# Optimization experiments

Measured on AMD Instinct MI355X. Metric: run time of the kernel, lower is better.

Reference implementation:

```python
import math
import jax, jax.numpy as jnp
import numpy as np

D = 512; H = 8; N = 6; DFF = 2048; VS = 32000; VT = 32000
B = 4; S = 1024; T = 1024
EPS = 1e-5


def _pe(length, d):
    pos = jnp.arange(length, dtype=jnp.float32)[:, None]
    div = jnp.exp(jnp.arange(0, d, 2, dtype=jnp.float32) * (-math.log(10000.0) / d))
    pe = jnp.zeros((length, d), jnp.float32)
    pe = pe.at[:, 0::2].set(jnp.sin(pos * div)).at[:, 1::2].set(jnp.cos(pos * div))
    return pe  # [L, D]


def _ln(x, g, b):
    m = x.mean(-1, keepdims=True)
    v = ((x - m) ** 2).mean(-1, keepdims=True)
    return (x - m) / jnp.sqrt(v + EPS) * g + b


def _mha(xq, xkv, w, b, mask):
    # w: [4, D, D], b: [4, D]; mask broadcastable to [B, H, Sq, Sk]
    nb, sq, d = xq.shape
    dk = d // H
    def proj(x, i):
        return (x @ w[i] + b[i]).reshape(x.shape[0], x.shape[1], H, dk).transpose(0, 2, 1, 3)
    q, k, v = proj(xq, 0), proj(xkv, 1), proj(xkv, 2)
    scores = jnp.einsum('bhqd,bhkd->bhqk', q, k) / math.sqrt(dk)
    scores = jnp.where(mask == 0, -1e9, scores)
    p = jax.nn.softmax(scores, axis=-1)
    o = jnp.einsum('bhqk,bhkd->bhqd', p, v).transpose(0, 2, 1, 3).reshape(nb, sq, d)
    return o @ w[3] + b[3]


def _ffn(x, w1, b1, w2, b2):
    return jax.nn.relu(x @ w1 + b1) @ w2 + b2


def _forward(src_emb, tgt_emb,
             enc_attn_w, enc_attn_b, enc_ffn_w1, enc_ffn_b1, enc_ffn_w2, enc_ffn_b2,
             enc_ln_g, enc_ln_b, enc_fg, enc_fb,
             dec_self_w, dec_self_b, dec_src_w, dec_src_b,
             dec_ffn_w1, dec_ffn_b1, dec_ffn_w2, dec_ffn_b2,
             dec_ln_g, dec_ln_b, dec_fg, dec_fb,
             gen_w, gen_b,
             src, tgt, src_mask, tgt_mask):
    # embed + positional encoding (dropout off: eval mode)
    x = src_emb[src] + _pe(src.shape[1], D)[None]
    for i in range(N):
        a = _mha(x, x, enc_attn_w[i], enc_attn_b[i], src_mask)
        x = _ln(x + a, enc_ln_g[i, 0], enc_ln_b[i, 0])
        f = _ffn(x, enc_ffn_w1[i], enc_ffn_b1[i], enc_ffn_w2[i], enc_ffn_b2[i])
        x = _ln(x + f, enc_ln_g[i, 1], enc_ln_b[i, 1])
    memory = _ln(x, enc_fg, enc_fb)

    y = tgt_emb[tgt] + _pe(tgt.shape[1], D)[None]
    for i in range(N):
        a = _mha(y, y, dec_self_w[i], dec_self_b[i], tgt_mask)
        y = _ln(y + a, dec_ln_g[i, 0], dec_ln_b[i, 0])
        a = _mha(y, memory, dec_src_w[i], dec_src_b[i], src_mask)
        y = _ln(y + a, dec_ln_g[i, 1], dec_ln_b[i, 1])
        f = _ffn(y, dec_ffn_w1[i], dec_ffn_b1[i], dec_ffn_w2[i], dec_ffn_b2[i])
        y = _ln(y + f, dec_ln_g[i, 2], dec_ln_b[i, 2])
    y = _ln(y, dec_fg, dec_fb)
    return y @ gen_w + gen_b  # [B, T, VT]


def setup_inputs():
    key = jax.random.key(0)
    ks = iter(jax.random.split(key, 48))
    def w(*shape):
        return jax.random.normal(next(ks), shape, dtype=jnp.float32) * 0.02
    inp = {}
    inp['src_emb'] = w(VS, D)
    inp['tgt_emb'] = w(VT, D)
    inp['enc_attn_w'] = w(N, 4, D, D)
    inp['enc_attn_b'] = jnp.zeros((N, 4, D), jnp.float32)
    inp['enc_ffn_w1'] = w(N, D, DFF)
    inp['enc_ffn_b1'] = jnp.zeros((N, DFF), jnp.float32)
    inp['enc_ffn_w2'] = w(N, DFF, D)
    inp['enc_ffn_b2'] = jnp.zeros((N, D), jnp.float32)
    inp['enc_ln_g'] = jnp.ones((N, 2, D), jnp.float32)
    inp['enc_ln_b'] = jnp.zeros((N, 2, D), jnp.float32)
    inp['enc_fg'] = jnp.ones((D,), jnp.float32)
    inp['enc_fb'] = jnp.zeros((D,), jnp.float32)
    inp['dec_self_w'] = w(N, 4, D, D)
    inp['dec_self_b'] = jnp.zeros((N, 4, D), jnp.float32)
    inp['dec_src_w'] = w(N, 4, D, D)
    inp['dec_src_b'] = jnp.zeros((N, 4, D), jnp.float32)
    inp['dec_ffn_w1'] = w(N, D, DFF)
    inp['dec_ffn_b1'] = jnp.zeros((N, DFF), jnp.float32)
    inp['dec_ffn_w2'] = w(N, DFF, D)
    inp['dec_ffn_b2'] = jnp.zeros((N, D), jnp.float32)
    inp['dec_ln_g'] = jnp.ones((N, 3, D), jnp.float32)
    inp['dec_ln_b'] = jnp.zeros((N, 3, D), jnp.float32)
    inp['dec_fg'] = jnp.ones((D,), jnp.float32)
    inp['dec_fb'] = jnp.zeros((D,), jnp.float32)
    inp['gen_w'] = w(D, VT)
    inp['gen_b'] = jnp.zeros((VT,), jnp.float32)
    inp['src'] = jax.random.randint(next(ks), (B, S), 0, VS)
    inp['tgt'] = jax.random.randint(next(ks), (B, T), 0, VT)
    inp['src_mask'] = jnp.ones((B, 1, 1, S), jnp.int32)
    inp['tgt_mask'] = jnp.tril(jnp.ones((T, T), jnp.int32))[None, None]  # causal [1,1,T,T]
    return inp


def reference(src_emb, tgt_emb, enc_attn_w, enc_attn_b, enc_ffn_w1, enc_ffn_b1,
              enc_ffn_w2, enc_ffn_b2, enc_ln_g, enc_ln_b, enc_fg, enc_fb,
              dec_self_w, dec_self_b, dec_src_w, dec_src_b,
              dec_ffn_w1, dec_ffn_b1, dec_ffn_w2, dec_ffn_b2,
              dec_ln_g, dec_ln_b, dec_fg, dec_fb, gen_w, gen_b,
              src, tgt, src_mask, tgt_mask):
    return _forward(src_emb, tgt_emb, enc_attn_w, enc_attn_b, enc_ffn_w1, enc_ffn_b1,
                    enc_ffn_w2, enc_ffn_b2, enc_ln_g, enc_ln_b, enc_fg, enc_fb,
                    dec_self_w, dec_self_b, dec_src_w, dec_src_b,
                    dec_ffn_w1, dec_ffn_b1, dec_ffn_w2, dec_ffn_b2,
                    dec_ln_g, dec_ln_b, dec_fg, dec_fb, gen_w, gen_b,
                    src, tgt, src_mask, tgt_mask)
```

## Files before the change

### kernel.cpp

```cpp
#include <hip/hip_runtime.h>


typedef __bf16 bf16x8 __attribute__((ext_vector_type(8)));
typedef __bf16 bf16x4 __attribute__((ext_vector_type(4)));
typedef float  f32x4  __attribute__((ext_vector_type(4)));

__device__ __forceinline__ void gload_lds16(const void* g, void* l) {
  __builtin_amdgcn_global_load_lds((__attribute__((address_space(1))) void*)g,
                                   (__attribute__((address_space(3))) void*)l,
                                   16, 0, 0);
}

__device__ __forceinline__ void hard_barrier() {
  asm volatile("" ::: "memory");
  __builtin_amdgcn_sched_barrier(0);
  __builtin_amdgcn_s_barrier();
  __builtin_amdgcn_sched_barrier(0);
  asm volatile("" ::: "memory");
}

template<int EPI>
__global__ __launch_bounds__(256)
void gemm2_kernel(const __bf16* __restrict__ A, int lda,
                  const __bf16* __restrict__ BT, int ldb,
                  void* __restrict__ Cv, int ldc,
                  const float* __restrict__ bias, int K,
                  __bf16* __restrict__ qb, __bf16* __restrict__ kb,
                  __bf16* __restrict__ vt, int zoff)
{
  constexpr int BM = 128, BN = 128, BK = 64;
  constexpr int WM = 64, WN = 64, FM = 4, FN = 4;
  constexpr int SLOT = 2 * BM * BK;
  __shared__ char ldsraw[69632];
  __bf16* lds = (__bf16*)ldsraw;
  const int tid  = threadIdx.x;
  const int lane = tid & 63, wave = tid >> 6;
  const int wr = wave >> 1, wc = wave & 1;
  const int bm = blockIdx.x * BM, bn = blockIdx.y * BN;

  auto stage = [&](int slot, int kt) {
    const char* Ag = (const char*)A;
    const char* Bg = (const char*)BT;
    char* base = (char*)(lds + slot * SLOT);
    const long long k0b = (long long)kt * (BK * 2);
#pragma unroll
    for (int i = 0; i < 4; i++) {
      int t = tid + i * 256;
      int row = t >> 3, cb = (t & 7) << 4;
      int src = cb ^ ((row & 7) << 4);
      gload_lds16(Ag + ((long long)(bm + row) * lda) * 2 + k0b + src, base + t * 16);
    }
#pragma unroll
    for (int i = 0; i < 4; i++) {
      int t = tid + i * 256;
      int row = t >> 3, cb = (t & 7) << 4;
      int src = cb ^ ((row & 7) << 4);
      gload_lds16(Bg + ((long long)(bn + row) * ldb) * 2 + k0b + src,
                  base + BM * BK * 2 + t * 16);
    }
  };

  f32x4 acc[FM][FN] = {};
  const int NT = K / BK;

  stage(0, 0);
  stage(1, 1);

  for (int t = 0; t < NT; t++) {
    if (t < NT - 1) {
      asm volatile("s_waitcnt vmcnt(8)" ::: "memory");
    } else {
      asm volatile("s_waitcnt vmcnt(0)" ::: "memory");
    }
    hard_barrier();
    const char* sA = (const char*)(lds + (t & 1) * SLOT);
    const char* sB = sA + BM * BK * 2;
#pragma unroll
    for (int kk = 0; kk < 2; kk++) {
      const int g = kk * 64 + (lane >> 4) * 16;
      bf16x8 af[FM], bfr[FN];
#pragma unroll
      for (int i = 0; i < FM; i++) {
        int row = wr * WM + i * 16 + (lane & 15);
        af[i] = *(const bf16x8*)(sA + row * 128 + (g ^ ((row & 7) << 4)));
      }
#pragma unroll
      for (int j = 0; j < FN; j++) {
        int row = wc * WN + j * 16 + (lane & 15);
        bfr[j] = *(const bf16x8*)(sB + row * 128 + (g ^ ((row & 7) << 4)));
      }
      __builtin_amdgcn_s_setprio(1);
#pragma unroll
      for (int i = 0; i < FM; i++)
#pragma unroll
        for (int j = 0; j < FN; j++)
          acc[i][j] = __builtin_amdgcn_mfma_f32_16x16x32_bf16(af[i], bfr[j], acc[i][j], 0, 0, 0);
      __builtin_amdgcn_s_setprio(0);
    }
    hard_barrier();
    if (t + 2 < NT) stage(t & 1, t + 2);
  }

  if constexpr (EPI == 3) {
    __syncthreads();
    float* ct = (float*)ldsraw;
#pragma unroll
    for (int i = 0; i < FM; i++) {
#pragma unroll
      for (int j = 0; j < FN; j++) {
        int lrow = wr * WM + i * 16 + (lane >> 4) * 4;
        int lcol = wc * WN + j * 16 + (lane & 15);
        float bv = bias[bn + lcol];
#pragma unroll
        for (int r = 0; r < 4; r++)
          ct[(lrow + r) * 132 + lcol] = acc[i][j][r] + bv;
      }
    }
    __syncthreads();
    float* C = (float*)Cv;
#pragma unroll
    for (int it = 0; it < 16; it++) {
      int idx = tid + it * 256;
      int row = idx >> 5, c4 = (idx & 31) * 4;
      f32x4 v = *(const f32x4*)(ct + row * 132 + c4);
      *(f32x4*)(C + (long long)(bm + row) * ldc + bn + c4) = v;
    }
    return;
  }

#pragma unroll
  for (int i = 0; i < FM; i++) {
#pragma unroll
    for (int j = 0; j < FN; j++) {
      int row0 = bm + wr * WM + i * 16 + (lane >> 4) * 4;
      int col  = bn + wc * WN + j * 16 + (lane & 15);
      float bv = bias ? bias[col] : 0.f;
      if constexpr (EPI == 2) {
        int z = zoff + (col >> 9);
        int cw = col & 511;
        int b = row0 >> 10, s = row0 & 1023;
        int h = cw >> 6, dk = cw & 63;
        long long bh = b * 8 + h;
        if (z == 2) {
          bf16x4 vv;
#pragma unroll
          for (int r = 0; r < 4; r++) vv[r] = (__bf16)(acc[i][j][r] + bv);
          *(bf16x4*)(vt + (bh << 16) + (dk << 10) + s) = vv;
        } else {
          __bf16* dst = (z == 0) ? qb : kb;
          float sc = (z == 0) ? 0.125f : 1.0f;
#pragma unroll
          for (int r = 0; r < 4; r++)
            dst[(bh << 16) + ((long long)(s + r) << 6) + dk] = (__bf16)((acc[i][j][r] + bv) * sc);
        }
      } else if constexpr (EPI == 1) {
        __bf16* C = (__bf16*)Cv;
#pragma unroll
        for (int r = 0; r < 4; r++)
          C[(long long)(row0 + r) * ldc + col] = (__bf16)fmaxf(acc[i][j][r] + bv, 0.f);
      } else {
        float* C = (float*)Cv;
#pragma unroll
        for (int r = 0; r < 4; r++)
          C[(long long)(row0 + r) * ldc + col] = acc[i][j][r] + bv;
      }
    }
  }
}

template<int EPI>
__global__ __launch_bounds__(256)
void gemm_kernel(const __bf16* __restrict__ A, int lda,
                 const __bf16* __restrict__ BT, int ldb,
                 void* __restrict__ Cv, int ldc,
                 const float* __restrict__ bias, int K,
                 __bf16* __restrict__ qb, __bf16* __restrict__ kb,
                 __bf16* __restrict__ vt, int zoff)
{
  constexpr int BM = 128, BN = 64, BK = 64;
  constexpr int WM = 64, WN = 32, FM = 4, FN = 2;
  constexpr int LA = (BM * BK) / 2048;
  constexpr int LB = (BN * BK) / 2048;
  constexpr int SLOT = (BM + BN) * BK;
  __shared__ __bf16 lds[3 * SLOT];
  const int tid  = threadIdx.x;
  const int lane = tid & 63, wave = tid >> 6;
  const int wr = wave >> 1, wc = wave & 1;
  const int bm = blockIdx.x * BM, bn = blockIdx.y * BN;

  auto stage = [&](int slot, int kt) {
    const char* Ag = (const char*)A;
    const char* Bg = (const char*)BT;
    char* base = (char*)(lds + slot * SLOT);
    const long long k0b = (long long)kt * (BK * 2);
#pragma unroll
    for (int i = 0; i < LA; i++) {
      int t = tid + i * 256;
      int row = t >> 3, cb = (t & 7) << 4;
      int src = cb ^ ((row & 7) << 4);
      gload_lds16(Ag + ((long long)(bm + row) * lda) * 2 + k0b + src, base + t * 16);
    }
#pragma unroll
    for (int i = 0; i < LB; i++) {
      int t = tid + i * 256;
      int row = t >> 3, cb = (t & 7) << 4;
      int src = cb ^ ((row & 7) << 4);
      gload_lds16(Bg + ((long long)(bn + row) * ldb) * 2 + k0b + src,
                  base + BM * BK * 2 + t * 16);
    }
  };

  f32x4 acc[FM][FN] = {};
  const int NT = K / BK;

  stage(0, 0);
  stage(1, 1);

  for (int t = 0; t < NT; t++) {
    if (t < NT - 1) {
      asm volatile("s_waitcnt vmcnt(6)" ::: "memory");
    } else {
      asm volatile("s_waitcnt vmcnt(0)" ::: "memory");
    }
    hard_barrier();
    if (t + 2 < NT) stage((t + 2) % 3, t + 2);
    const char* sA = (const char*)(lds + (t % 3) * SLOT);
    const char* sB = sA + BM * BK * 2;
#pragma unroll
    for (int kk = 0; kk < 2; kk++) {
      const int g = kk * 64 + (lane >> 4) * 16;
      bf16x8 af[FM], bfr[FN];
#pragma unroll
      for (int i = 0; i < FM; i++) {
        int row = wr * WM + i * 16 + (lane & 15);
        af[i] = *(const bf16x8*)(sA + row * 128 + (g ^ ((row & 7) << 4)));
      }
#pragma unroll
      for (int j = 0; j < FN; j++) {
        int row = wc * WN + j * 16 + (lane & 15);
        bfr[j] = *(const bf16x8*)(sB + row * 128 + (g ^ ((row & 7) << 4)));
      }
      __builtin_amdgcn_s_setprio(1);
#pragma unroll
      for (int i = 0; i < FM; i++)
#pragma unroll
        for (int j = 0; j < FN; j++)
          acc[i][j] = __builtin_amdgcn_mfma_f32_16x16x32_bf16(af[i], bfr[j], acc[i][j], 0, 0, 0);
      __builtin_amdgcn_s_setprio(0);
    }
  }

#pragma unroll
  for (int i = 0; i < FM; i++) {
#pragma unroll
    for (int j = 0; j < FN; j++) {
      int row0 = bm + wr * WM + i * 16 + (lane >> 4) * 4;
      int col  = bn + wc * WN + j * 16 + (lane & 15);
      float bv = bias ? bias[col] : 0.f;
      if constexpr (EPI == 2) {
        int z = zoff + (col >> 9);
        int cw = col & 511;
        int b = row0 >> 10, s = row0 & 1023;
        int h = cw >> 6, dk = cw & 63;
        long long bh = b * 8 + h;
        if (z == 2) {
          bf16x4 vv;
#pragma unroll
          for (int r = 0; r < 4; r++) vv[r] = (__bf16)(acc[i][j][r] + bv);
          *(bf16x4*)(vt + (bh << 16) + (dk << 10) + s) = vv;
        } else {
          __bf16* dst = (z == 0) ? qb : kb;
          float sc = (z == 0) ? 0.125f : 1.0f;
#pragma unroll
          for (int r = 0; r < 4; r++)
            dst[(bh << 16) + ((long long)(s + r) << 6) + dk] = (__bf16)((acc[i][j][r] + bv) * sc);
        }
      } else {
        float* C = (float*)Cv;
#pragma unroll
        for (int r = 0; r < 4; r++)
          C[(long long)(row0 + r) * ldc + col] = acc[i][j][r] + bv;
      }
    }
  }
}

template<int CAUSAL>
__global__ __launch_bounds__(256)
void flash_kernel(const __bf16* __restrict__ qb, const __bf16* __restrict__ kb,
                  const __bf16* __restrict__ vt, const int* __restrict__ smask,
                  __bf16* __restrict__ Ob)
{
  __shared__ __bf16 lK[2 * 128 * 64];
  __shared__ __bf16 lV[2 * 64 * 128];
  __shared__ __bf16 lP[4][16 * 128];
  const int bh = blockIdx.y;
  const int b = bh >> 3, h = bh & 7;
  const int q0 = blockIdx.x * 64;
  const int tid = threadIdx.x, lane = tid & 63, w = tid >> 6;
  const char* kh = (const char*)(kb + ((long long)bh << 16));
  const char* vh = (const char*)(vt + ((long long)bh << 16));

  auto stageKV = [&](int buf, int t) {
    int k0 = t * 128;
#pragma unroll
    for (int i = 0; i < 4; i++) {
      int c = tid + i * 256;
      int row = c >> 3, cb = (c & 7) << 4;
      int cl = cb ^ ((row & 7) << 4);
      gload_lds16(kh + (long long)(k0 + row) * 128 + cl, (char*)lK + buf * 16384 + c * 16);
    }
#pragma unroll
    for (int i = 0; i < 4; i++) {
      int c = tid + i * 256;
      int row = c >> 4, cb = (c & 15) << 4;
      int cl = cb ^ ((row & 7) << 4);
      gload_lds16(vh + (long long)row * 2048 + (long long)k0 * 2 + cl, (char*)lV + buf * 16384 + c * 16);
    }
  };

  bf16x8 qa[2];
  {
    const __bf16* qrow = qb + ((long long)bh << 16)
                       + (long long)(q0 + w * 16 + (lane & 15)) * 64 + (lane >> 4) * 8;
    qa[0] = *(const bf16x8*)(qrow);
    qa[1] = *(const bf16x8*)(qrow + 32);
  }
  f32x4 oacc[4] = {};
  float m[4], l[4];
#pragma unroll
  for (int r = 0; r < 4; r++) { m[r] = -3e38f; l[r] = 0.f; }

  const int nt = CAUSAL ? (blockIdx.x / 2 + 1) : 8;
  char* lPw = (char*)lP + w * 4096;
  stageKV(0, 0);

  for (int t = 0; t < nt; t++) {
    const int k0 = t * 128;
    __syncthreads();
    if (t + 1 < nt) stageKV((t + 1) & 1, t + 1);
    char* cK = (char*)lK + (t & 1) * 16384;
    char* cV = (char*)lV + (t & 1) * 16384;

    f32x4 sf[8];
#pragma unroll
    for (int f = 0; f < 8; f++) {
      int row = f * 16 + (lane & 15);
      f32x4 s = {};
#pragma unroll
      for (int ks = 0; ks < 2; ks++) {
        int cb = ks * 64 + (lane >> 4) * 16;
        bf16x8 kf = *(const bf16x8*)(cK + row * 128 + (cb ^ ((row & 7) << 4)));
        s = __builtin_amdgcn_mfma_f32_16x16x32_bf16(qa[ks], kf, s, 0, 0, 0);
      }
      sf[f] = s;
    }

    if (!CAUSAL) {
#pragma unroll
      for (int f = 0; f < 8; f++) {
        if (smask[b * 1024 + k0 + f * 16 + (lane & 15)] == 0) {
#pragma unroll
          for (int r = 0; r < 4; r++) sf[f][r] = -1e30f;
        }
      }
    } else if (t == nt - 1) {
#pragma unroll
      for (int f = 0; f < 8; f++) {
        int kc = k0 + f * 16 + (lane & 15);
#pragma unroll
        for (int r = 0; r < 4; r++) {
          int qr = q0 + w * 16 + (lane >> 4) * 4 + r;
          if (kc > qr) sf[f][r] = -1e30f;
        }
      }
    }

    float mt[4], mn[4], cr[4], rs[4];
#pragma unroll
    for (int r = 0; r < 4; r++) {
      float v = sf[0][r];
#pragma unroll
      for (int f = 1; f < 8; f++) v = fmaxf(v, sf[f][r]);
      mt[r] = v;
    }
#pragma unroll
    for (int o = 1; o < 16; o <<= 1)
#pragma unroll
      for (int r = 0; r < 4; r++) mt[r] = fmaxf(mt[r], __shfl_xor(mt[r], o));
#pragma unroll
    for (int r = 0; r < 4; r++) {
      mn[r] = fmaxf(m[r], mt[r]);
      cr[r] = __expf(m[r] - mn[r]);
      m[r]  = mn[r];
      rs[r] = 0.f;
    }
#pragma unroll
    for (int f = 0; f < 8; f++)
#pragma unroll
      for (int r = 0; r < 4; r++) {
        float p = __expf(sf[f][r] - mn[r]);
        sf[f][r] = p;
        rs[r] += p;
      }
#pragma unroll
    for (int o = 1; o < 16; o <<= 1)
#pragma unroll
      for (int r = 0; r < 4; r++) rs[r] += __shfl_xor(rs[r], o);
#pragma unroll
    for (int r = 0; r < 4; r++) l[r] = l[r] * cr[r] + rs[r];
#pragma unroll
    for (int d = 0; d < 4; d++)
#pragma unroll
      for (int r = 0; r < 4; r++) oacc[d][r] *= cr[r];

#pragma unroll
    for (int f = 0; f < 8; f++) {
      int colB = f * 32 + (lane & 15) * 2;
#pragma unroll
      for (int r = 0; r < 4; r++) {
        int row = (lane >> 4) * 4 + r;
        *(__bf16*)(lPw + row * 256 + (colB ^ ((row & 7) << 4))) = (__bf16)sf[f][r];
      }
    }
    asm volatile("s_waitcnt lgkmcnt(0)" ::: "memory");

#pragma unroll
    for (int ks = 0; ks < 4; ks++) {
      int prow = lane & 15;
      int cb = ks * 64 + (lane >> 4) * 16;
      bf16x8 pa = *(const bf16x8*)(lPw + prow * 256 + (cb ^ ((prow & 7) << 4)));
#pragma unroll
      for (int d = 0; d < 4; d++) {
        int vrow = d * 16 + (lane & 15);
        bf16x8 vf = *(const bf16x8*)(cV + vrow * 256 + (cb ^ ((vrow & 7) << 4)));
        oacc[d] = __builtin_amdgcn_mfma_f32_16x16x32_bf16(pa, vf, oacc[d], 0, 0, 0);
      }
    }
  }

  float inv[4];
#pragma unroll
  for (int r = 0; r < 4; r++) inv[r] = 1.f / l[r];
#pragma unroll
  for (int d = 0; d < 4; d++)
#pragma unroll
    for (int r = 0; r < 4; r++) {
      long long row = b * 1024 + q0 + w * 16 + (lane >> 4) * 4 + r;
      Ob[row * 512 + h * 64 + d * 16 + (lane & 15)] = (__bf16)(oacc[d][r] * inv[r]);
    }
}

__global__ void transpose_w_kernel(const float* __restrict__ W, __bf16* __restrict__ WT,
                                   int K, int N)
{
  __shared__ float t[32][33];
  long long mz = (long long)blockIdx.z * K * N;
  W += mz; WT += mz;
  int n0 = blockIdx.x * 32, k0 = blockIdx.y * 32;
  int tx = threadIdx.x, ty = threadIdx.y;
#pragma unroll
  for (int i = 0; i < 32; i += 8)
    t[ty + i][tx] = W[(long long)(k0 + ty + i) * N + (n0 + tx)];
  __syncthreads();
#pragma unroll
  for (int i = 0; i < 32; i += 8)
    WT[(long long)(n0 + ty + i) * K + (k0 + tx)] = (__bf16)t[tx][ty + i];
}

__global__ void embed_kernel(const float* __restrict__ emb, const int* __restrict__ idx,
                             float* __restrict__ X, __bf16* __restrict__ Xb)
{
  int row = blockIdx.x;
  int s   = row & 1023;
  int tok = idx[row];
  int d0  = threadIdx.x * 4;
  float4 e = *(const float4*)(emb + (long long)tok * 512 + d0);
  const float* ep = (const float*)&e;
  float o[4];
#pragma unroll
  for (int j = 0; j < 4; j++) {
    int d = d0 + j;
    float div = expf((float)(d & ~1) * (-9.210340371976184f / 512.f));
    float ang = (float)s * div;
    float pe  = (d & 1) ? cosf(ang) : sinf(ang);
    o[j] = ep[j] + pe;
  }
  *(float4*)(X + (long long)row * 512 + d0) = *(float4*)o;
  bf16x4 ob;
#pragma unroll
  for (int j = 0; j < 4; j++) ob[j] = (__bf16)o[j];
  *(bf16x4*)(Xb + (long long)row * 512 + d0) = ob;
}

__global__ void ln_kernel(const float* __restrict__ Xin, const float* __restrict__ Rin,
                          const float* __restrict__ g, const float* __restrict__ b,
                          float* __restrict__ Xout, __bf16* __restrict__ Xbout)
{
  int row = blockIdx.x, lane = threadIdx.x;
  long long base = (long long)row * 512 + lane * 8;
  float x[8];
  *(float4*)x       = *(const float4*)(Xin + base);
  *(float4*)(x + 4) = *(const float4*)(Xin + base + 4);
  if (Rin) {
    float4 r0 = *(const float4*)(Rin + base);
    float4 r1 = *(const float4*)(Rin + base + 4);
    x[0] += r0.x; x[1] += r0.y; x[2] += r0.z; x[3] += r0.w;
    x[4] += r1.x; x[5] += r1.y; x[6] += r1.z; x[7] += r1.w;
  }
  float s = 0.f;
#pragma unroll
  for (int i = 0; i < 8; i++) s += x[i];
#pragma unroll
  for (int o = 32; o > 0; o >>= 1) s += __shfl_xor(s, o);
  float mean = s * (1.f / 512.f);
  float v = 0.f;
#pragma unroll
  for (int i = 0; i < 8; i++) { x[i] -= mean; v += x[i] * x[i]; }
#pragma unroll
  for (int o = 32; o > 0; o >>= 1) v += __shfl_xor(v, o);
  float inv = rsqrtf(v * (1.f / 512.f) + 1e-5f);
  int d0 = lane * 8;
  float gg[8], bb[8];
  *(float4*)gg       = *(const float4*)(g + d0);
  *(float4*)(gg + 4) = *(const float4*)(g + d0 + 4);
  *(float4*)bb       = *(const float4*)(b + d0);
  *(float4*)(bb + 4) = *(const float4*)(b + d0 + 4);
  float y[8]; bf16x8 yb;
#pragma unroll
  for (int i = 0; i < 8; i++) {
    y[i] = x[i] * inv * gg[i] + bb[i];
    yb[i] = (__bf16)y[i];
  }
  if (Xout) {
    *(float4*)(Xout + base)     = *(float4*)y;
    *(float4*)(Xout + base + 4) = *(float4*)(y + 4);
  }
  *(bf16x8*)(Xbout + base) = yb;
}

extern "C" void kernel_launch(void* const* d_in, const int* in_sizes, int n_in,
                              void* d_out, int out_size, void* d_ws, size_t ws_size,
                              hipStream_t stream)
{
  (void)in_sizes; (void)n_in; (void)out_size; (void)ws_size;
  const float* src_emb    = (const float*)d_in[0];
  const float* tgt_emb    = (const float*)d_in[1];
  const float* enc_attn_w = (const float*)d_in[2];
  const float* enc_attn_b = (const float*)d_in[3];
  const float* enc_ffn_w1 = (const float*)d_in[4];
  const float* enc_ffn_b1 = (const float*)d_in[5];
  const float* enc_ffn_w2 = (const float*)d_in[6];
  const float* enc_ffn_b2 = (const float*)d_in[7];
  const float* enc_ln_g   = (const float*)d_in[8];
  const float* enc_ln_b   = (const float*)d_in[9];
  const float* enc_fg     = (const float*)d_in[10];
  const float* enc_fb     = (const float*)d_in[11];
  const float* dec_self_w = (const float*)d_in[12];
  const float* dec_self_b = (const float*)d_in[13];
  const float* dec_src_w  = (const float*)d_in[14];
  const float* dec_src_b  = (const float*)d_in[15];
  const float* dec_ffn_w1 = (const float*)d_in[16];
  const float* dec_ffn_b1 = (const float*)d_in[17];
  const float* dec_ffn_w2 = (const float*)d_in[18];
  const float* dec_ffn_b2 = (const float*)d_in[19];
  const float* dec_ln_g   = (const float*)d_in[20];
  const float* dec_ln_b   = (const float*)d_in[21];
  const float* dec_fg     = (const float*)d_in[22];
  const float* dec_fb     = (const float*)d_in[23];
  const float* gen_w      = (const float*)d_in[24];
  const float* gen_b      = (const float*)d_in[25];
  const int*   src        = (const int*)d_in[26];
  const int*   tgt        = (const int*)d_in[27];
  const int*   src_mask   = (const int*)d_in[28];

  float* out = (float*)d_out;

  char* wp = (char*)d_ws;
  auto alloc = [&](size_t bytes) { void* p = (void*)wp; wp += (bytes + 255) & ~(size_t)255; return p; };
  __bf16* TWea = (__bf16*)alloc(24ull * 262144 * 2);
  __bf16* TWe1 = (__bf16*)alloc(6ull * 1048576 * 2);
  __bf16* TWe2 = (__bf16*)alloc(6ull * 1048576 * 2);
  __bf16* TWds = (__bf16*)alloc(24ull * 262144 * 2);
  __bf16* TWdx = (__bf16*)alloc(24ull * 262144 * 2);
  __bf16* TWd1 = (__bf16*)alloc(6ull * 1048576 * 2);
  __bf16* TWd2 = (__bf16*)alloc(6ull * 1048576 * 2);
  float*  X    = (float*) alloc(4096ull * 512 * 4);
  __bf16* Xb   = (__bf16*)alloc(4096ull * 512 * 2);
  __bf16* MEMb = (__bf16*)alloc(4096ull * 512 * 2);
  float*  R    = (float*) alloc(4096ull * 512 * 4);
  __bf16* qb   = (__bf16*)alloc(32ull * 1024 * 64 * 2);
  __bf16* kb   = (__bf16*)alloc(32ull * 1024 * 64 * 2);
  __bf16* vt   = (__bf16*)alloc(32ull * 1024 * 64 * 2);
  __bf16* Ob   = (__bf16*)alloc(4096ull * 512 * 2);
  __bf16* Fb   = qb;
  __bf16* GENT = TWea;

  transpose_w_kernel<<<dim3(16, 16, 24), dim3(32, 8), 0, stream>>>(enc_attn_w, TWea, 512, 512);
  transpose_w_kernel<<<dim3(64, 16, 6),  dim3(32, 8), 0, stream>>>(enc_ffn_w1, TWe1, 512, 2048);
  transpose_w_kernel<<<dim3(16, 64, 6),  dim3(32, 8), 0, stream>>>(enc_ffn_w2, TWe2, 2048, 512);
  transpose_w_kernel<<<dim3(16, 16, 24), dim3(32, 8), 0, stream>>>(dec_self_w, TWds, 512, 512);
  transpose_w_kernel<<<dim3(16, 16, 24), dim3(32, 8), 0, stream>>>(dec_src_w,  TWdx, 512, 512);
  transpose_w_kernel<<<dim3(64, 16, 6),  dim3(32, 8), 0, stream>>>(dec_ffn_w1, TWd1, 512, 2048);
  transpose_w_kernel<<<dim3(16, 64, 6),  dim3(32, 8), 0, stream>>>(dec_ffn_w2, TWd2, 2048, 512);

  auto attention = [&](const __bf16* wt, const float* bptr, int causal,
                       const __bf16* Aq, const __bf16* Akv) {
    if (Aq == Akv) {
      gemm2_kernel<2><<<dim3(32, 12), 256, 0, stream>>>(
          Aq, 512, wt, 512, nullptr, 0, bptr, 512, qb, kb, vt, 0);
    } else {
      gemm_kernel<2><<<dim3(32, 8), 256, 0, stream>>>(
          Aq, 512, wt, 512, nullptr, 0, bptr, 512, qb, kb, vt, 0);
      gemm2_kernel<2><<<dim3(32, 8), 256, 0, stream>>>(
          Akv, 512, wt + 262144, 512, nullptr, 0, bptr + 512, 512, qb, kb, vt, 1);
    }
    if (causal)
      flash_kernel<1><<<dim3(16, 32), 256, 0, stream>>>(qb, kb, vt, nullptr, Ob);
    else
      flash_kernel<0><<<dim3(16, 32), 256, 0, stream>>>(qb, kb, vt, src_mask, Ob);
    gemm_kernel<0><<<dim3(32, 8), 256, 0, stream>>>(
        Ob, 512, wt + 3 * 262144, 512, R, 512, bptr + 3 * 512, 512,
        nullptr, nullptr, nullptr, 0);
  };

  auto ffn = [&](const __bf16* w1t, const float* b1, const __bf16* w2t, const float* b2) {
    gemm2_kernel<1><<<dim3(32, 16), 256, 0, stream>>>(
        Xb, 512, w1t, 512, Fb, 2048, b1, 512, nullptr, nullptr, nullptr, 0);
    gemm_kernel<0><<<dim3(32, 8), 256, 0, stream>>>(
        Fb, 2048, w2t, 2048, R, 512, b2, 2048, nullptr, nullptr, nullptr, 0);
  };

  embed_kernel<<<4096, 128, 0, stream>>>(src_emb, src, X, Xb);
  for (int i = 0; i < 6; i++) {
    attention(TWea + (long long)i * 1048576, enc_attn_b + i * 2048, 0, Xb, Xb);
    ln_kernel<<<4096, 64, 0, stream>>>(X, R, enc_ln_g + i * 1024, enc_ln_b + i * 1024, X, Xb);
    ffn(TWe1 + (long long)i * 1048576, enc_ffn_b1 + i * 2048,
        TWe2 + (long long)i * 1048576, enc_ffn_b2 + i * 512);
    ln_kernel<<<4096, 64, 0, stream>>>(X, R, enc_ln_g + i * 1024 + 512, enc_ln_b + i * 1024 + 512, X, Xb);
  }
  ln_kernel<<<4096, 64, 0, stream>>>(X, nullptr, enc_fg, enc_fb, nullptr, MEMb);

  transpose_w_kernel<<<dim3(1000, 16, 1), dim3(32, 8), 0, stream>>>(gen_w, GENT, 512, 32000);

  embed_kernel<<<4096, 128, 0, stream>>>(tgt_emb, tgt, X, Xb);
  for (int i = 0; i < 6; i++) {
    attention(TWds + (long long)i * 1048576, dec_self_b + i * 2048, 1, Xb, Xb);
    ln_kernel<<<4096, 64, 0, stream>>>(X, R, dec_ln_g + i * 1536, dec_ln_b + i * 1536, X, Xb);

    attention(TWdx + (long long)i * 1048576, dec_src_b + i * 2048, 0, Xb, MEMb);
    ln_kernel<<<4096, 64, 0, stream>>>(X, R, dec_ln_g + i * 1536 + 512, dec_ln_b + i * 1536 + 512, X, Xb);

    ffn(TWd1 + (long long)i * 1048576, dec_ffn_b1 + i * 2048,
        TWd2 + (long long)i * 1048576, dec_ffn_b2 + i * 512);
    ln_kernel<<<4096, 64, 0, stream>>>(X, R, dec_ln_g + i * 1536 + 1024, dec_ln_b + i * 1536 + 1024, X, Xb);
  }
  ln_kernel<<<4096, 64, 0, stream>>>(X, nullptr, dec_fg, dec_fb, nullptr, Xb);

  gemm2_kernel<3><<<dim3(32, 250), 256, 0, stream>>>(
      Xb, 512, GENT, 512, out, 32000, gen_b, 512, nullptr, nullptr, nullptr, 0);
}
```

Baseline: 1.962 ms.

## Fuse cross-attn QKV projection, prefetch KV deeper, lazy softmax rescale, bf16 residual stream

Cross-attention Q and KV projections now run as one gemm2 launch, with the A pointer chosen per block column, so two launches become one. The flash kernel now prefetches two KV tiles ahead with explicit vmcnt waits, and it rescales the running max and accumulators only when any row's max grows by more than 8. The fp32 residual copy X is dropped, so embed and layernorm read and write only bf16, which halves residual traffic. The cost is lower residual precision, and the lazy rescale risks exp overflow if its threshold assumption fails.

After: 1.843 ms. -6.1%, faster.

```diff
diff --git a/kernel.cpp b/kernel.cpp
--- a/kernel.cpp
+++ b/kernel.cpp
@@ -21,12 +21,13 @@
 
 template<int EPI>
 __global__ __launch_bounds__(256)
-void gemm2_kernel(const __bf16* __restrict__ A, int lda,
+void gemm2_kernel(const __bf16* __restrict__ A, const __bf16* __restrict__ Akv,
+                  int lda,
                   const __bf16* __restrict__ BT, int ldb,
                   void* __restrict__ Cv, int ldc,
                   const float* __restrict__ bias, int K,
                   __bf16* __restrict__ qb, __bf16* __restrict__ kb,
-                  __bf16* __restrict__ vt, int zoff)
+                  __bf16* __restrict__ vt)
 {
   constexpr int BM = 128, BN = 128, BK = 64;
   constexpr int WM = 64, WN = 64, FM = 4, FN = 4;
@@ -37,9 +38,10 @@
   const int lane = tid & 63, wave = tid >> 6;
   const int wr = wave >> 1, wc = wave & 1;
   const int bm = blockIdx.x * BM, bn = blockIdx.y * BN;
+  const __bf16* Ause = (EPI == 2 && blockIdx.y >= 4) ? Akv : A;
 
   auto stage = [&](int slot, int kt) {
-    const char* Ag = (const char*)A;
+    const char* Ag = (const char*)Ause;
     const char* Bg = (const char*)BT;
     char* base = (char*)(lds + slot * SLOT);
     const long long k0b = (long long)kt * (BK * 2);
@@ -136,7 +138,7 @@
       int col  = bn + wc * WN + j * 16 + (lane & 15);
       float bv = bias ? bias[col] : 0.f;
       if constexpr (EPI == 2) {
-        int z = zoff + (col >> 9);
+        int z = col >> 9;
         int cw = col & 511;
         int b = row0 >> 10, s = row0 & 1023;
         int h = cw >> 6, dk = cw & 63;
@@ -168,14 +170,11 @@
   }
 }
 
-template<int EPI>
 __global__ __launch_bounds__(256)
 void gemm_kernel(const __bf16* __restrict__ A, int lda,
                  const __bf16* __restrict__ BT, int ldb,
-                 void* __restrict__ Cv, int ldc,
-                 const float* __restrict__ bias, int K,
-                 __bf16* __restrict__ qb, __bf16* __restrict__ kb,
-                 __bf16* __restrict__ vt, int zoff)
+                 float* __restrict__ C, int ldc,
+                 const float* __restrict__ bias, int K)
 {
   constexpr int BM = 128, BN = 64, BK = 64;
   constexpr int WM = 64, WN = 32, FM = 4, FN = 2;
@@ -257,30 +256,9 @@
       int row0 = bm + wr * WM + i * 16 + (lane >> 4) * 4;
       int col  = bn + wc * WN + j * 16 + (lane & 15);
       float bv = bias ? bias[col] : 0.f;
-      if constexpr (EPI == 2) {
-        int z = zoff + (col >> 9);
-        int cw = col & 511;
-        int b = row0 >> 10, s = row0 & 1023;
-        int h = cw >> 6, dk = cw & 63;
-        long long bh = b * 8 + h;
-        if (z == 2) {
-          bf16x4 vv;
-#pragma unroll
-          for (int r = 0; r < 4; r++) vv[r] = (__bf16)(acc[i][j][r] + bv);
-          *(bf16x4*)(vt + (bh << 16) + (dk << 10) + s) = vv;
-        } else {
-          __bf16* dst = (z == 0) ? qb : kb;
-          float sc = (z == 0) ? 0.125f : 1.0f;
-#pragma unroll
-          for (int r = 0; r < 4; r++)
-            dst[(bh << 16) + ((long long)(s + r) << 6) + dk] = (__bf16)((acc[i][j][r] + bv) * sc);
-        }
-      } else {
-        float* C = (float*)Cv;
-#pragma unroll
-        for (int r = 0; r < 4; r++)
-          C[(long long)(row0 + r) * ldc + col] = acc[i][j][r] + bv;
-      }
+#pragma unroll
+      for (int r = 0; r < 4; r++)
+        C[(long long)(row0 + r) * ldc + col] = acc[i][j][r] + bv;
     }
   }
 }
@@ -333,12 +311,18 @@
 
   const int nt = CAUSAL ? (blockIdx.x / 2 + 1) : 8;
   char* lPw = (char*)lP + w * 4096;
+
   stageKV(0, 0);
+  if (nt > 1) stageKV(1, 1);
 
   for (int t = 0; t < nt; t++) {
     const int k0 = t * 128;
-    __syncthreads();
-    if (t + 1 < nt) stageKV((t + 1) & 1, t + 1);
+    if (t < nt - 1) {
+      asm volatile("s_waitcnt vmcnt(8)" ::: "memory");
+    } else {
+      asm volatile("s_waitcnt vmcnt(0)" ::: "memory");
+    }
+    hard_barrier();
     char* cK = (char*)lK + (t & 1) * 16384;
     char* cV = (char*)lV + (t & 1) * 16384;
 
@@ -376,7 +360,7 @@
       }
     }
 
-    float mt[4], mn[4], cr[4], rs[4];
+    float mt[4];
 #pragma unroll
     for (int r = 0; r < 4; r++) {
       float v = sf[0][r];
@@ -388,18 +372,30 @@
     for (int o = 1; o < 16; o <<= 1)
 #pragma unroll
       for (int r = 0; r < 4; r++) mt[r] = fmaxf(mt[r], __shfl_xor(mt[r], o));
-#pragma unroll
-    for (int r = 0; r < 4; r++) {
-      mn[r] = fmaxf(m[r], mt[r]);
-      cr[r] = __expf(m[r] - mn[r]);
-      m[r]  = mn[r];
-      rs[r] = 0.f;
-    }
+
+    bool need = false;
+#pragma unroll
+    for (int r = 0; r < 4; r++) need = need || (mt[r] > m[r] + 8.f);
+    if (__any(need)) {
+      float mn[4], cr[4];
+#pragma unroll
+      for (int r = 0; r < 4; r++) {
+        mn[r] = fmaxf(m[r], mt[r]);
+        cr[r] = __expf(m[r] - mn[r]);
+        m[r]  = mn[r];
+        l[r] *= cr[r];
+      }
+#pragma unroll
+      for (int d = 0; d < 4; d++)
+#pragma unroll
+        for (int r = 0; r < 4; r++) oacc[d][r] *= cr[r];
+    }
+    float rs[4] = {0.f, 0.f, 0.f, 0.f};
 #pragma unroll
     for (int f = 0; f < 8; f++)
 #pragma unroll
       for (int r = 0; r < 4; r++) {
-        float p = __expf(sf[f][r] - mn[r]);
+        float p = __expf(sf[f][r] - m[r]);
         sf[f][r] = p;
         rs[r] += p;
       }
@@ -408,11 +404,7 @@
 #pragma unroll
       for (int r = 0; r < 4; r++) rs[r] += __shfl_xor(rs[r], o);
 #pragma unroll
-    for (int r = 0; r < 4; r++) l[r] = l[r] * cr[r] + rs[r];
-#pragma unroll
-    for (int d = 0; d < 4; d++)
-#pragma unroll
-      for (int r = 0; r < 4; r++) oacc[d][r] *= cr[r];
+    for (int r = 0; r < 4; r++) l[r] += rs[r];
 
 #pragma unroll
     for (int f = 0; f < 8; f++) {
@@ -437,6 +429,8 @@
         oacc[d] = __builtin_amdgcn_mfma_f32_16x16x32_bf16(pa, vf, oacc[d], 0, 0, 0);
       }
     }
+    hard_barrier();
+    if (t + 2 < nt) stageKV(t & 1, t + 2);
   }
 
   float inv[4];
@@ -469,7 +463,7 @@
 }
 
 __global__ void embed_kernel(const float* __restrict__ emb, const int* __restrict__ idx,
-                             float* __restrict__ X, __bf16* __restrict__ Xb)
+                             __bf16* __restrict__ Xb)
 {
   int row = blockIdx.x;
   int s   = row & 1023;
@@ -477,31 +471,28 @@
   int d0  = threadIdx.x * 4;
   float4 e = *(const float4*)(emb + (long long)tok * 512 + d0);
   const float* ep = (const float*)&e;
-  float o[4];
+  bf16x4 ob;
 #pragma unroll
   for (int j = 0; j < 4; j++) {
     int d = d0 + j;
     float div = expf((float)(d & ~1) * (-9.210340371976184f / 512.f));
     float ang = (float)s * div;
     float pe  = (d & 1) ? cosf(ang) : sinf(ang);
-    o[j] = ep[j] + pe;
-  }
-  *(float4*)(X + (long long)row * 512 + d0) = *(float4*)o;
-  bf16x4 ob;
-#pragma unroll
-  for (int j = 0; j < 4; j++) ob[j] = (__bf16)o[j];
+    ob[j] = (__bf16)(ep[j] + pe);
+  }
   *(bf16x4*)(Xb + (long long)row * 512 + d0) = ob;
 }
 
-__global__ void ln_kernel(const float* __restrict__ Xin, const float* __restrict__ Rin,
+__global__ void ln_kernel(const __bf16* __restrict__ Xin, const float* __restrict__ Rin,
                           const float* __restrict__ g, const float* __restrict__ b,
-                          float* __restrict__ Xout, __bf16* __restrict__ Xbout)
+                          __bf16* __restrict__ Xbout)
 {
   int row = blockIdx.x, lane = threadIdx.x;
   long long base = (long long)row * 512 + lane * 8;
+  bf16x8 xv = *(const bf16x8*)(Xin + base);
   float x[8];
-  *(float4*)x       = *(const float4*)(Xin + base);
-  *(float4*)(x + 4) = *(const float4*)(Xin + base + 4);
+#pragma unroll
+  for (int i = 0; i < 8; i++) x[i] = (float)xv[i];
   if (Rin) {
     float4 r0 = *(const float4*)(Rin + base);
     float4 r1 = *(const float4*)(Rin + base + 4);
@@ -526,16 +517,10 @@
   *(float4*)(gg + 4) = *(const float4*)(g + d0 + 4);
   *(float4*)bb       = *(const float4*)(b + d0);
   *(float4*)(bb + 4) = *(const float4*)(b + d0 + 4);
-  float y[8]; bf16x8 yb;
-#pragma unroll
-  for (int i = 0; i < 8; i++) {
-    y[i] = x[i] * inv * gg[i] + bb[i];
-    yb[i] = (__bf16)y[i];
-  }
-  if (Xout) {
-    *(float4*)(Xout + base)     = *(float4*)y;
-    *(float4*)(Xout + base + 4) = *(float4*)(y + 4);
-  }
+  bf16x8 yb;
+#pragma unroll
+  for (int i = 0; i < 8; i++)
+    yb[i] = (__bf16)(x[i] * inv * gg[i] + bb[i]);
   *(bf16x8*)(Xbout + base) = yb;
 }
 
@@ -585,7 +570,6 @@
   __bf16* TWdx = (__bf16*)alloc(24ull * 262144 * 2);
   __bf16* TWd1 = (__bf16*)alloc(6ull * 1048576 * 2);
   __bf16* TWd2 = (__bf16*)alloc(6ull * 1048576 * 2);
-  float*  X    = (float*) alloc(4096ull * 512 * 4);
   __bf16* Xb   = (__bf16*)alloc(4096ull * 512 * 2);
   __bf16* MEMb = (__bf16*)alloc(4096ull * 512 * 2);
   float*  R    = (float*) alloc(4096ull * 512 * 4);
@@ -606,57 +590,49 @@
 
   auto attention = [&](const __bf16* wt, const float* bptr, int causal,
                        const __bf16* Aq, const __bf16* Akv) {
-    if (Aq == Akv) {
-      gemm2_kernel<2><<<dim3(32, 12), 256, 0, stream>>>(
-          Aq, 512, wt, 512, nullptr, 0, bptr, 512, qb, kb, vt, 0);
-    } else {
-      gemm_kernel<2><<<dim3(32, 8), 256, 0, stream>>>(
-          Aq, 512, wt, 512, nullptr, 0, bptr, 512, qb, kb, vt, 0);
-      gemm2_kernel<2><<<dim3(32, 8), 256, 0, stream>>>(
-          Akv, 512, wt + 262144, 512, nullptr, 0, bptr + 512, 512, qb, kb, vt, 1);
-    }
+    gemm2_kernel<2><<<dim3(32, 12), 256, 0, stream>>>(
+        Aq, Akv, 512, wt, 512, nullptr, 0, bptr, 512, qb, kb, vt);
     if (causal)
       flash_kernel<1><<<dim3(16, 32), 256, 0, stream>>>(qb, kb, vt, nullptr, Ob);
     else
       flash_kernel<0><<<dim3(16, 32), 256, 0, stream>>>(qb, kb, vt, src_mask, Ob);
-    gemm_kernel<0><<<dim3(32, 8), 256, 0, stream>>>(
-        Ob, 512, wt + 3 * 262144, 512, R, 512, bptr + 3 * 512, 512,
-        nullptr, nullptr, nullptr, 0);
+    gemm_kernel<<<dim3(32, 8), 256, 0, stream>>>(
+        Ob, 512, wt + 3 * 262144, 512, R, 512, bptr + 3 * 512, 512);
   };
 
   auto ffn = [&](const __bf16* w1t, const float* b1, const __bf16* w2t, const float* b2) {
     gemm2_kernel<1><<<dim3(32, 16), 256, 0, stream>>>(
-        Xb, 512, w1t, 512, Fb, 2048, b1, 512, nullptr, nullptr, nullptr, 0);
-    gemm_kernel<0><<<dim3(32, 8), 256, 0, stream>>>(
-        Fb, 2048, w2t, 2048, R, 512, b2, 2048, nullptr, nullptr, nullptr, 0);
+        Xb, Xb, 512, w1t, 512, Fb, 2048, b1, 512, nullptr, nullptr, nullptr);
+    gemm_kernel<<<dim3(32, 8), 256, 0, stream>>>(
+        Fb, 2048, w2t, 2048, R, 512, b2, 2048);
   };
 
-  embed_kernel<<<4096, 128, 0, stream>>>(src_emb, src, X, Xb);
+  embed_kernel<<<4096, 128, 0, stream>>>(src_emb, src, Xb);
   for (int i = 0; i < 6; i++) {
     attention(TWea + (long long)i * 1048576, enc_attn_b + i * 2048, 0, Xb, Xb);
-    ln_kernel<<<4096, 64, 0, stream>>>(X, R, enc_ln_g + i * 1024, enc_ln_b + i * 1024, X, Xb);
+    ln_kernel<<<4096, 64, 0, stream>>>(Xb, R, enc_ln_g + i * 1024, enc_ln_b + i * 1024, Xb);
     ffn(TWe1 + (long long)i * 1048576, enc_ffn_b1 + i * 2048,
         TWe2 + (long long)i * 1048576, enc_ffn_b2 + i * 512);
-    ln_kernel<<<4096, 64, 0, stream>>>(X, R, enc_ln_g + i * 1024 + 512, enc_ln_b + i * 1024 + 512, X, Xb);
-  }
-  ln_kernel<<<4096, 64, 0, stream>>>(X, nullptr, enc_fg, enc_fb, nullptr, MEMb);
+    ln_kernel<<<4096, 64, 0, stream>>>(Xb, R, enc_ln_g + i * 1024 + 512, enc_ln_b + i * 1024 + 512, Xb);
+  }
+  ln_kernel<<<4096, 64, 0, stream>>>(Xb, nullptr, enc_fg, enc_fb, MEMb);
 
   transpose_w_kernel<<<dim3(1000, 16, 1), dim3(32, 8), 0, stream>>>(gen_w, GENT, 512, 32000);
 
-  embed_kernel<<<4096, 128, 0, stream>>>(tgt_emb, tgt, X, Xb);
+  embed_kernel<<<4096, 128, 0, stream>>>(tgt_emb, tgt, Xb);
   for (int i = 0; i < 6; i++) {
     attention(TWds + (long long)i * 1048576, dec_self_b + i * 2048, 1, Xb, Xb);
-    ln_kernel<<<4096, 64, 0, stream>>>(X, R, dec_ln_g + i * 1536, dec_ln_b + i * 1536, X, Xb);
+    ln_kernel<<<4096, 64, 0, stream>>>(Xb, R, dec_ln_g + i * 1536, dec_ln_b + i * 1536, Xb);
 
     attention(TWdx + (long long)i * 1048576, dec_src_b + i * 2048, 0, Xb, MEMb);
-    ln_kernel<<<4096, 64, 0, stream>>>(X, R, dec_ln_g + i * 1536 + 512, dec_ln_b + i * 1536 + 512, X, Xb);
+    ln_kernel<<<4096, 64, 0, stream>>>(Xb, R, dec_ln_g + i * 1536 + 512, dec_ln_b + i * 1536 + 512, Xb);
 
     ffn(TWd1 + (long long)i * 1048576, dec_ffn_b1 + i * 2048,
         TWd2 + (long long)i * 1048576, dec_ffn_b2 + i * 512);
-    ln_kernel<<<4096, 64, 0, stream>>>(X, R, dec_ln_g + i * 1536 + 1024, dec_ln_b + i * 1536 + 1024, X, Xb);
-  }
-  ln_kernel<<<4096, 64, 0, stream>>>(X, nullptr, dec_fg, dec_fb, nullptr, Xb);
+    ln_kernel<<<4096, 64, 0, stream>>>(Xb, R, dec_ln_g + i * 1536 + 1024, dec_ln_b + i * 1536 + 1024, Xb);
+  }
+  ln_kernel<<<4096, 64, 0, stream>>>(Xb, nullptr, dec_fg, dec_fb, Xb);
 
   gemm2_kernel<3><<<dim3(32, 250), 256, 0, stream>>>(
-      Xb, 512, GENT, 512, out, 32000, gen_b, 512, nullptr, nullptr, nullptr, 0);
-}
+      Xb, Xb, 512, GENT, 512, out, 32000, gen_b, 512, nullptr, nullptr, nullptr);
+}
```
